# Kernel tuning notes

Measured on AMD Instinct MI355X. Metric: run time of the kernel, lower is better.

## Reference

```python
import jax, jax.numpy as jnp
import numpy as np
from jax import lax

NUM_HEADS = 4
NUM_GROUPS = 32
EPS = 1e-5


def group_norm(x, gamma, beta):
    # x: [b, c, t]
    b, c, t = x.shape
    xg = x.reshape(b, NUM_GROUPS, c // NUM_GROUPS, t)
    mu = jnp.mean(xg, axis=(2, 3), keepdims=True)
    var = jnp.var(xg, axis=(2, 3), keepdims=True)
    xg = (xg - mu) * lax.rsqrt(var + EPS)
    x = xg.reshape(b, c, t)
    return x * gamma[None, :, None] + beta[None, :, None]


def conv1d_same(x, w, b):
    # x: [b, c_in, t], w: [c_out, c_in, k] -> TF-style SAME padding, stride 1
    k = w.shape[-1]
    left = (k - 1) // 2
    right = (k - 1) - left
    y = lax.conv_general_dilated(x, w, window_strides=(1,),
                                 padding=[(left, right)],
                                 dimension_numbers=('NCH', 'OIH', 'NCH'))
    return y + b[None, :, None]


def qkv_attention(qkv):
    # qkv: [b*heads, 3*ch, t]
    ch = qkv.shape[1] // 3
    q, k, v = jnp.split(qkv, 3, axis=1)
    scale = float(ch) ** -0.25  # 1/sqrt(sqrt(ch)) applied to both q and k
    w = jnp.einsum('bct,bcs->bts', q * scale, k * scale)
    w = jax.nn.softmax(w.astype(jnp.float32), axis=-1).astype(qkv.dtype)
    return jnp.einsum('bts,bcs->bct', w, v)


def setup_inputs() -> dict:
    key = jax.random.key(0)
    ks = jax.random.split(key, 5)
    B, C, H, W = 4, 512, 64, 64
    x = jax.random.normal(ks[0], (B, C, H, W), dtype=jnp.float32)
    gn_gamma = jnp.ones((C,), dtype=jnp.float32)
    gn_beta = jnp.zeros((C,), dtype=jnp.float32)
    qkv_w = jax.random.normal(ks[1], (3 * C, C, C // 16), dtype=jnp.float32) * 0.02
    qkv_b = jax.random.normal(ks[2], (3 * C,), dtype=jnp.float32) * 0.02
    proj_w = jax.random.normal(ks[3], (C, C, 5), dtype=jnp.float32) * 0.02
    proj_b = jax.random.normal(ks[4], (C,), dtype=jnp.float32) * 0.02
    return {"x": x, "gn_gamma": gn_gamma, "gn_beta": gn_beta,
            "qkv_w": qkv_w, "qkv_b": qkv_b, "proj_w": proj_w, "proj_b": proj_b}


def reference(x, gn_gamma, gn_beta, qkv_w, qkv_b, proj_w, proj_b):
    b, c = x.shape[0], x.shape[1]
    spatial = x.shape[2:]
    t = int(np.prod(spatial))
    xf = x.reshape(b, c, t)
    qkv = conv1d_same(group_norm(xf, gn_gamma, gn_beta), qkv_w, qkv_b)  # [b, 3c, t]
    qkv = qkv.reshape(b * NUM_HEADS, -1, t)
    h = qkv_attention(qkv)               # [b*heads, c//heads, t]
    h = h.reshape(b, -1, t)              # [b, c, t]
    h = conv1d_same(h, proj_w, proj_b)
    return (xf + h).reshape(b, c, *spatial)
```

## Files before the change

kernel.cpp:

```cpp
#include <hip/hip_runtime.h>
#include <hip/hip_bf16.h>
#include <math.h>

typedef __attribute__((ext_vector_type(8))) __bf16 bf16x8;
typedef __attribute__((ext_vector_type(4))) float  f32x4;

__device__ __forceinline__ unsigned short f2bf(float f) {
    union { float f; unsigned int u; } x; x.f = f;
    unsigned int r = x.u + 0x7fffu + ((x.u >> 16) & 1u);
    return (unsigned short)(r >> 16);
}

__device__ __forceinline__ void gl_lds16(const unsigned short* g, unsigned short* l) {
    auto gp = (const unsigned int __attribute__((address_space(1)))*)((const void*)g);
    auto lp = (unsigned int __attribute__((address_space(3)))*)(unsigned int)(unsigned long long)((void*)l);
    __builtin_amdgcn_global_load_lds(gp, lp, 16, 0, 0);
}

#define B_   4
#define C_   512
#define T_   4096
#define NH   4
#define DH   128

__global__ __launch_bounds__(256) void cvt_wqkv(const float* __restrict__ w, unsigned short* __restrict__ o) {
    __shared__ unsigned short l[512 * 33];
    int co = blockIdx.x;
    const float* src = w + (size_t)co * 16384;
    for (int j = 0; j < 64; j++) {
        int i = threadIdx.x + j * 256;
        l[(i >> 5) * 33 + (i & 31)] = f2bf(src[i]);
    }
    __syncthreads();
    unsigned short* dst = o + (size_t)co * 16384;
    for (int j = 0; j < 64; j++) {
        int i = threadIdx.x + j * 256;
        int dk = i >> 9, ci = i & 511;
        dst[i] = l[ci * 33 + dk];
    }
}

__global__ __launch_bounds__(256) void cvt_wproj(const float* __restrict__ w, unsigned short* __restrict__ o) {
    __shared__ unsigned short l[512 * 6];
    int co = blockIdx.x;
    const float* src = w + (size_t)co * 2560;
    for (int j = 0; j < 10; j++) {
        int i = threadIdx.x + j * 256;
        int ci = i / 5, dk = i - ci * 5;
        l[ci * 6 + dk] = f2bf(src[i]);
    }
    __syncthreads();
    unsigned short* dst = o + (size_t)co * 2560;
    for (int j = 0; j < 10; j++) {
        int i = threadIdx.x + j * 256;
        int dk = i >> 9, ci = i & 511;
        dst[i] = l[ci * 6 + dk];
    }
}

__global__ __launch_bounds__(1024) void groupnorm(const float* __restrict__ x,
                                                  const float* __restrict__ gamma,
                                                  const float* __restrict__ beta,
                                                  unsigned short* __restrict__ gnT) {
    int g = blockIdx.x, b = blockIdx.y;
    int tid = threadIdx.x;
    const float* base = x + ((size_t)b * C_ + g * 16) * T_;
    float s = 0.f, s2 = 0.f;
    const float4* b4 = (const float4*)base;
    for (int j = 0; j < 16; j++) {
        float4 v = b4[tid + j * 1024];
        s  += v.x + v.y + v.z + v.w;
        s2 += v.x * v.x + v.y * v.y + v.z * v.z + v.w * v.w;
    }
    for (int off = 32; off; off >>= 1) { s += __shfl_down(s, off, 64); s2 += __shfl_down(s2, off, 64); }
    __shared__ float red[34];
    int wid = tid >> 6, lane = tid & 63;
    if (lane == 0) { red[wid] = s; red[16 + wid] = s2; }
    __syncthreads();
    if (tid == 0) {
        float ts = 0.f, ts2 = 0.f;
        for (int i = 0; i < 16; i++) { ts += red[i]; ts2 += red[16 + i]; }
        float mu = ts / 65536.f;
        float var = ts2 / 65536.f - mu * mu;
        red[32] = mu; red[33] = rsqrtf(var + 1e-5f);
    }
    __syncthreads();
    float mu = red[32], inv = red[33];
    for (int p = 0; p < 4; p++) {
        int t = tid + p * 1024;
        unsigned short outv[16];
        for (int cc = 0; cc < 16; cc++) {
            float xv = base[(size_t)cc * T_ + t];
            int c = g * 16 + cc;
            outv[cc] = f2bf((xv - mu) * inv * gamma[c] + beta[c]);
        }
        unsigned short* dst = gnT + ((size_t)b * T_ + t) * C_ + g * 16;
        *(uint4*)dst       = *(uint4*)outv;
        *(uint4*)(dst + 8) = *(uint4*)(outv + 8);
    }
}

__global__ __launch_bounds__(256, 3) void gemm_qkv(const unsigned short* __restrict__ gnT,
                                                   const unsigned short* __restrict__ wq,
                                                   const float* __restrict__ bias,
                                                   unsigned short* __restrict__ qT,
                                                   unsigned short* __restrict__ kT,
                                                   unsigned short* __restrict__ vv) {
    int nblk = blockIdx.x, mblk = blockIdx.y, b = blockIdx.z;
    int m0 = mblk * 128, t0 = nblk * 128;
    __shared__ unsigned short As[128 * 64];
    __shared__ unsigned short Bs[128 * 64];
    int tid = threadIdx.x, lane = tid & 63, wave = tid >> 6;
    int quad = lane >> 4, l16 = lane & 15;
    int wm = wave & 1, wn = wave >> 1;

    int srow8 = lane >> 3;
    int scb = (lane & 7) ^ srow8;
    const unsigned short* gb = gnT + (size_t)b * T_ * C_;
    const unsigned short* ap[4]; const unsigned short* bp[4];
    unsigned short *la[4], *lb[4];
#pragma unroll
    for (int i = 0; i < 4; i++) {
        int g = wave * 4 + i;
        int row = g * 8 + srow8;
        ap[i] = wq + (size_t)(m0 + row) * 16384 + scb * 8;
        bp[i] = gb + ((size_t)(t0 - 15 + row)) * 512 + scb * 8;
        la[i] = As + g * 512;
        lb[i] = Bs + g * 512;
    }
    const unsigned short* pAr[2]; const unsigned short* pBr[2];
#pragma unroll
    for (int kk = 0; kk < 2; kk++) {
        pAr[kk] = As + (wm * 64 + l16) * 64 + (((kk * 4 + quad) ^ (l16 & 7)) << 3);
        pBr[kk] = Bs + (wn * 64 + l16) * 64 + (((kk * 4 + quad) ^ (l16 & 7)) << 3);
    }
    f32x4 acc[4][4];
    f32x4 z4 = {0.f, 0.f, 0.f, 0.f};
#pragma unroll
    for (int mt = 0; mt < 4; mt++)
#pragma unroll
        for (int nt = 0; nt < 4; nt++) acc[mt][nt] = z4;

    bool isF = (nblk == 0), isL = (nblk == 31);
    for (int s = 0; s < 256; s++) {
        __syncthreads();
#pragma unroll
        for (int i = 0; i < 4; i++) { gl_lds16(ap[i], la[i]); ap[i] += 64; }
#pragma unroll
        for (int i = 0; i < 4; i++) { gl_lds16(bp[i], lb[i]); bp[i] += 64; }
        __syncthreads();
        int dk = s >> 3;
        if (isF && dk < 15) {
            int nz = 15 - dk, r = tid >> 3;
            if (r < nz) *(uint4*)&Bs[(r << 6) + ((tid & 7) << 3)] = make_uint4(0, 0, 0, 0);
            __syncthreads();
        }
        if (isL && dk > 15) {
            int nb = dk - 15, rr = tid >> 3;
            if (rr < nb) *(uint4*)&Bs[((128 - nb + rr) << 6) + ((tid & 7) << 3)] = make_uint4(0, 0, 0, 0);
            __syncthreads();
        }
#pragma unroll
        for (int kk = 0; kk < 2; kk++) {
            bf16x8 af[4], bfr[4];
#pragma unroll
            for (int mt = 0; mt < 4; mt++) af[mt]  = *(const bf16x8*)(pAr[kk] + mt * 1024);
#pragma unroll
            for (int nt = 0; nt < 4; nt++) bfr[nt] = *(const bf16x8*)(pBr[kk] + nt * 1024);
#pragma unroll
            for (int mt = 0; mt < 4; mt++)
#pragma unroll
                for (int nt = 0; nt < 4; nt++)
                    acc[mt][nt] = __builtin_amdgcn_mfma_f32_16x16x32_bf16(af[mt], bfr[nt], acc[mt][nt], 0, 0, 0);
        }
    }
#pragma unroll
    for (int mt = 0; mt < 4; mt++) {
        int cobase = m0 + wm * 64 + mt * 16 + quad * 4;
        int h = cobase / 384;
        int local = cobase - h * 384;
        int bh = b * NH + h;
#pragma unroll
        for (int nt = 0; nt < 4; nt++) {
            int t = t0 + wn * 64 + nt * 16 + l16;
            f32x4 a = acc[mt][nt];
            unsigned short r4[4];
            for (int r = 0; r < 4; r++) r4[r] = f2bf(a[r] + bias[cobase + r]);
            if (local < 128) {
                unsigned short* dst = qT + ((size_t)bh * T_ + t) * DH + local;
                *(uint2*)dst = *(uint2*)r4;
            } else if (local < 256) {
                unsigned short* dst = kT + ((size_t)bh * T_ + t) * DH + (local - 128);
                *(uint2*)dst = *(uint2*)r4;
            } else {
                unsigned short* dst = vv + ((size_t)bh * DH + (local - 256)) * T_ + t;
                for (int r = 0; r < 4; r++) dst[(size_t)r * T_] = r4[r];
            }
        }
    }
}

__global__ __launch_bounds__(256, 3) void attn(const unsigned short* __restrict__ qT,
                                               const unsigned short* __restrict__ kT,
                                               const unsigned short* __restrict__ vv,
                                               unsigned short* __restrict__ hT) {
    int q0 = blockIdx.x * 64, bh = blockIdx.y;
    int b = bh >> 2, h = bh & 3;
    __shared__ unsigned short Ks[64 * 128];
    __shared__ unsigned short Vs[128 * 64];
    __shared__ unsigned short Ps[64 * 72];
    int tid = threadIdx.x, lane = tid & 63, wave = tid >> 6, quad = lane >> 4, l16 = lane & 15;

    bf16x8 bq[4];
    {
        const unsigned short* qrow = qT + ((size_t)bh * T_ + q0 + wave * 16 + l16) * DH + quad * 8;
#pragma unroll
        for (int kk = 0; kk < 4; kk++) bq[kk] = *(const bf16x8*)(qrow + kk * 32);
    }

    const unsigned short* kbase = kT + (size_t)bh * T_ * DH;
    const unsigned short* vbase = vv + (size_t)bh * DH * T_;
    int krow_in = lane >> 4, kp = lane & 15;
    int vrow_in = lane >> 3, vp = lane & 7;

    float m_i = -1e30f, l_i = 0.f;
    f32x4 z4 = {0.f, 0.f, 0.f, 0.f};
    f32x4 o[8];
#pragma unroll
    for (int nt = 0; nt < 8; nt++) o[nt] = z4;
    const float scale2 = 0.08838834764831845f;

    for (int ts0 = 0; ts0 < T_; ts0 += 64) {
        __syncthreads();
#pragma unroll
        for (int i = 0; i < 4; i++) {
            int row = (wave * 4 + i) * 4 + krow_in;
            gl_lds16(kbase + ((size_t)(ts0 + row)) * DH + (((kp ^ (row & 7)) << 3)),
                     Ks + (wave * 4 + i) * 512);
        }
#pragma unroll
        for (int i = 0; i < 4; i++) {
            int row = (wave * 4 + i) * 8 + vrow_in;
            gl_lds16(vbase + (size_t)row * T_ + ts0 + (((vp ^ (row & 7)) << 3)),
                     Vs + (wave * 4 + i) * 512);
        }
        __syncthreads();

        f32x4 s[4];
#pragma unroll
        for (int mt = 0; mt < 4; mt++) s[mt] = z4;
#pragma unroll
        for (int kk = 0; kk < 4; kk++) {
            int pb = (((kk * 4 + quad) ^ (l16 & 7)) << 3);
#pragma unroll
            for (int mt = 0; mt < 4; mt++) {
                bf16x8 ak = *(const bf16x8*)&Ks[(mt * 16 + l16) * 128 + pb];
                s[mt] = __builtin_amdgcn_mfma_f32_16x16x32_bf16(ak, bq[kk], s[mt], 0, 0, 0);
            }
        }
        float mx = -1e30f;
#pragma unroll
        for (int mt = 0; mt < 4; mt++) {
            s[mt] *= scale2;
            mx = fmaxf(mx, fmaxf(fmaxf(s[mt][0], s[mt][1]), fmaxf(s[mt][2], s[mt][3])));
        }
        mx = fmaxf(mx, __shfl_xor(mx, 16, 64));
        mx = fmaxf(mx, __shfl_xor(mx, 32, 64));
        float mnew = fmaxf(m_i, mx);
        float alpha = __expf(m_i - mnew);
        float rs = 0.f;
#pragma unroll
        for (int mt = 0; mt < 4; mt++) {
#pragma unroll
            for (int r = 0; r < 4; r++) { float p = __expf(s[mt][r] - mnew); s[mt][r] = p; rs += p; }
        }
        rs += __shfl_xor(rs, 16, 64);
        rs += __shfl_xor(rs, 32, 64);
        m_i = mnew;
        l_i = l_i * alpha + rs;
#pragma unroll
        for (int mt = 0; mt < 4; mt++) {
            unsigned short t4[4];
#pragma unroll
            for (int r = 0; r < 4; r++) t4[r] = f2bf(s[mt][r]);
            *(uint2*)&Ps[(wave * 16 + l16) * 72 + mt * 16 + quad * 4] = *(uint2*)t4;
        }
        float a0 = __shfl(alpha, quad * 4 + 0, 64);
        float a1 = __shfl(alpha, quad * 4 + 1, 64);
        float a2 = __shfl(alpha, quad * 4 + 2, 64);
        float a3 = __shfl(alpha, quad * 4 + 3, 64);
        f32x4 av = {a0, a1, a2, a3};
#pragma unroll
        for (int nt = 0; nt < 8; nt++) o[nt] *= av;
#pragma unroll
        for (int kk = 0; kk < 2; kk++) {
            bf16x8 ap = *(const bf16x8*)&Ps[(wave * 16 + l16) * 72 + kk * 32 + quad * 8];
            int pb = (((kk * 4 + quad) ^ (l16 & 7)) << 3);
#pragma unroll
            for (int nt = 0; nt < 8; nt++) {
                bf16x8 bv = *(const bf16x8*)&Vs[(nt * 16 + l16) * 64 + pb];
                o[nt] = __builtin_amdgcn_mfma_f32_16x16x32_bf16(ap, bv, o[nt], 0, 0, 0);
            }
        }
    }
    float i0 = 1.f / __shfl(l_i, quad * 4 + 0, 64);
    float i1 = 1.f / __shfl(l_i, quad * 4 + 1, 64);
    float i2 = 1.f / __shfl(l_i, quad * 4 + 2, 64);
    float i3 = 1.f / __shfl(l_i, quad * 4 + 3, 64);
    f32x4 iv = {i0, i1, i2, i3};
#pragma unroll
    for (int r = 0; r < 4; r++) {
        int t = q0 + wave * 16 + quad * 4 + r;
        unsigned short* dst = hT + ((size_t)b * T_ + t) * C_ + h * DH;
#pragma unroll
        for (int nt = 0; nt < 8; nt++) dst[nt * 16 + l16] = f2bf(o[nt][r] * iv[r]);
    }
}

__global__ __launch_bounds__(256, 3) void gemm_proj(const unsigned short* __restrict__ hT,
                                                    const unsigned short* __restrict__ wp,
                                                    const float* __restrict__ bias,
                                                    const float* __restrict__ x,
                                                    float* __restrict__ out) {
    int nblk = blockIdx.x, mblk = blockIdx.y, b = blockIdx.z;
    int m0 = mblk * 128, t0 = nblk * 128;
    __shared__ unsigned short As[128 * 64], Bs[128 * 64];
    int tid = threadIdx.x, lane = tid & 63, wave = tid >> 6;
    int quad = lane >> 4, l16 = lane & 15;
    int wm = wave & 1, wn = wave >> 1;

    int srow8 = lane >> 3;
    int scb = (lane & 7) ^ srow8;
    const unsigned short* hb = hT + (size_t)b * T_ * C_;
    const unsigned short* ap[4]; const unsigned short* bp[4];
    unsigned short *la[4], *lb[4];
#pragma unroll
    for (int i = 0; i < 4; i++) {
        int g = wave * 4 + i;
        int row = g * 8 + srow8;
        ap[i] = wp + (size_t)(m0 + row) * 2560 + scb * 8;
        bp[i] = hb + ((size_t)(t0 - 2 + row)) * 512 + scb * 8;
        la[i] = As + g * 512;
        lb[i] = Bs + g * 512;
    }
    const unsigned short* pAr[2]; const unsigned short* pBr[2];
#pragma unroll
    for (int kk = 0; kk < 2; kk++) {
        pAr[kk] = As + (wm * 64 + l16) * 64 + (((kk * 4 + quad) ^ (l16 & 7)) << 3);
        pBr[kk] = Bs + (wn * 64 + l16) * 64 + (((kk * 4 + quad) ^ (l16 & 7)) << 3);
    }
    f32x4 acc[4][4];
    f32x4 z4 = {0.f, 0.f, 0.f, 0.f};
#pragma unroll
    for (int mt = 0; mt < 4; mt++)
#pragma unroll
        for (int nt = 0; nt < 4; nt++) acc[mt][nt] = z4;

    bool isF = (nblk == 0), isL = (nblk == 31);
    for (int s = 0; s < 40; s++) {
        __syncthreads();
#pragma unroll
        for (int i = 0; i < 4; i++) { gl_lds16(ap[i], la[i]); ap[i] += 64; }
#pragma unroll
        for (int i = 0; i < 4; i++) { gl_lds16(bp[i], lb[i]); bp[i] += 64; }
        __syncthreads();
        int dk = s >> 3;
        if (isF && dk < 2) {
            int nz = 2 - dk, r = tid >> 3;
            if (r < nz) *(uint4*)&Bs[(r << 6) + ((tid & 7) << 3)] = make_uint4(0, 0, 0, 0);
            __syncthreads();
        }
        if (isL && dk > 2) {
            int nb = dk - 2, rr = tid >> 3;
            if (rr < nb) *(uint4*)&Bs[((128 - nb + rr) << 6) + ((tid & 7) << 3)] = make_uint4(0, 0, 0, 0);
            __syncthreads();
        }
#pragma unroll
        for (int kk = 0; kk < 2; kk++) {
            bf16x8 af[4], bfr[4];
#pragma unroll
            for (int mt = 0; mt < 4; mt++) af[mt]  = *(const bf16x8*)(pAr[kk] + mt * 1024);
#pragma unroll
            for (int nt = 0; nt < 4; nt++) bfr[nt] = *(const bf16x8*)(pBr[kk] + nt * 1024);
#pragma unroll
            for (int mt = 0; mt < 4; mt++)
#pragma unroll
                for (int nt = 0; nt < 4; nt++)
                    acc[mt][nt] = __builtin_amdgcn_mfma_f32_16x16x32_bf16(af[mt], bfr[nt], acc[mt][nt], 0, 0, 0);
        }
    }
#pragma unroll
    for (int mt = 0; mt < 4; mt++) {
        int cobase = m0 + wm * 64 + mt * 16 + quad * 4;
#pragma unroll
        for (int nt = 0; nt < 4; nt++) {
            int t = t0 + wn * 64 + nt * 16 + l16;
            for (int r = 0; r < 4; r++) {
                int co = cobase + r;
                size_t idx = ((size_t)(b * C_ + co)) * T_ + t;
                out[idx] = acc[mt][nt][r] + bias[co] + x[idx];
            }
        }
    }
}

extern "C" void kernel_launch(void* const* d_in, const int* in_sizes, int n_in,
                              void* d_out, int out_size, void* d_ws, size_t ws_size,
                              hipStream_t stream) {
    const float* x      = (const float*)d_in[0];
    const float* gamma  = (const float*)d_in[1];
    const float* beta   = (const float*)d_in[2];
    const float* qkv_w  = (const float*)d_in[3];
    const float* qkv_b  = (const float*)d_in[4];
    const float* proj_w = (const float*)d_in[5];
    const float* proj_b = (const float*)d_in[6];
    float* out = (float*)d_out;
    char* ws = (char*)d_ws;

    unsigned short* wqkvT  = (unsigned short*)(ws);
    unsigned short* wprojT = (unsigned short*)(ws + 50331648);
    unsigned short* gnT    = (unsigned short*)(ws + 52953088);
    unsigned short* qTb    = (unsigned short*)(ws + 69730304);
    unsigned short* kTb    = (unsigned short*)(ws + 86507520);
    unsigned short* vb     = (unsigned short*)(ws + 103284736);
    unsigned short* hT     = gnT;

    hipLaunchKernelGGL(cvt_wqkv,  dim3(1536),      dim3(256),  0, stream, qkv_w, wqkvT);
    hipLaunchKernelGGL(cvt_wproj, dim3(512),       dim3(256),  0, stream, proj_w, wprojT);
    hipLaunchKernelGGL(groupnorm, dim3(32, 4),     dim3(1024), 0, stream, x, gamma, beta, gnT);
    hipLaunchKernelGGL(gemm_qkv,  dim3(32, 12, 4), dim3(256),  0, stream, gnT, wqkvT, qkv_b, qTb, kTb, vb);
    hipLaunchKernelGGL(attn,      dim3(64, 16),    dim3(256),  0, stream, qTb, kTb, vb, hT);
    hipLaunchKernelGGL(gemm_proj, dim3(32, 4, 4),  dim3(256),  0, stream, hT, wprojT, proj_b, x, out);
}
```

Measured before the change: 1.268 ms.

## Double-buffer GEMM LDS tiles and process two query tiles per attention wave

The two conv GEMMs now use double-buffered shared-memory tiles, so the next K-slice's global-to-LDS load is issued before the current slice's MFMAs and one barrier per step is dropped. Grid indexing is flattened so batch and time blocks share the x dimension. The attention kernel gives each wave 32 query rows (two 16-row tiles), so each K/V tile in LDS is reused across 128 queries per block and fewer blocks reload K/V. The cost is more LDS and registers, with occupancy bounds lowered from 3 to 2. The async load into the other buffer also relies on the single barrier per iteration for correctness, including around the boundary zero-fill writes.

Result: slower. 1.371 ms (+8.1%).

```diff
diff --git a/kernel.cpp b/kernel.cpp
--- a/kernel.cpp
+++ b/kernel.cpp
@@ -100,16 +100,16 @@
     }
 }
 
-__global__ __launch_bounds__(256, 3) void gemm_qkv(const unsigned short* __restrict__ gnT,
+__global__ __launch_bounds__(256, 2) void gemm_qkv(const unsigned short* __restrict__ gnT,
                                                    const unsigned short* __restrict__ wq,
                                                    const float* __restrict__ bias,
                                                    unsigned short* __restrict__ qT,
                                                    unsigned short* __restrict__ kT,
                                                    unsigned short* __restrict__ vv) {
-    int nblk = blockIdx.x, mblk = blockIdx.y, b = blockIdx.z;
+    int nblk = blockIdx.x & 31, b = blockIdx.x >> 5, mblk = blockIdx.y;
     int m0 = mblk * 128, t0 = nblk * 128;
-    __shared__ unsigned short As[128 * 64];
-    __shared__ unsigned short Bs[128 * 64];
+    __shared__ unsigned short As[2][128 * 64];
+    __shared__ unsigned short Bs[2][128 * 64];
     int tid = threadIdx.x, lane = tid & 63, wave = tid >> 6;
     int quad = lane >> 4, l16 = lane & 15;
     int wm = wave & 1, wn = wave >> 1;
@@ -118,22 +118,18 @@
     int scb = (lane & 7) ^ srow8;
     const unsigned short* gb = gnT + (size_t)b * T_ * C_;
     const unsigned short* ap[4]; const unsigned short* bp[4];
-    unsigned short *la[4], *lb[4];
+    int lo[4];
 #pragma unroll
     for (int i = 0; i < 4; i++) {
         int g = wave * 4 + i;
         int row = g * 8 + srow8;
         ap[i] = wq + (size_t)(m0 + row) * 16384 + scb * 8;
         bp[i] = gb + ((size_t)(t0 - 15 + row)) * 512 + scb * 8;
-        la[i] = As + g * 512;
-        lb[i] = Bs + g * 512;
-    }
-    const unsigned short* pAr[2]; const unsigned short* pBr[2];
-#pragma unroll
-    for (int kk = 0; kk < 2; kk++) {
-        pAr[kk] = As + (wm * 64 + l16) * 64 + (((kk * 4 + quad) ^ (l16 & 7)) << 3);
-        pBr[kk] = Bs + (wn * 64 + l16) * 64 + (((kk * 4 + quad) ^ (l16 & 7)) << 3);
-    }
+        lo[i] = g * 512;
+    }
+    int fo[2];
+#pragma unroll
+    for (int kk = 0; kk < 2; kk++) fo[kk] = (((kk * 4 + quad) ^ (l16 & 7)) << 3);
     f32x4 acc[4][4];
     f32x4 z4 = {0.f, 0.f, 0.f, 0.f};
 #pragma unroll
@@ -142,31 +138,39 @@
         for (int nt = 0; nt < 4; nt++) acc[mt][nt] = z4;
 
     bool isF = (nblk == 0), isL = (nblk == 31);
+#pragma unroll
+    for (int i = 0; i < 4; i++) { gl_lds16(ap[i], &As[0][lo[i]]); ap[i] += 64; }
+#pragma unroll
+    for (int i = 0; i < 4; i++) { gl_lds16(bp[i], &Bs[0][lo[i]]); bp[i] += 64; }
+
     for (int s = 0; s < 256; s++) {
+        int cur = s & 1;
         __syncthreads();
-#pragma unroll
-        for (int i = 0; i < 4; i++) { gl_lds16(ap[i], la[i]); ap[i] += 64; }
-#pragma unroll
-        for (int i = 0; i < 4; i++) { gl_lds16(bp[i], lb[i]); bp[i] += 64; }
-        __syncthreads();
+        if (s != 255) {
+            int nx = cur ^ 1;
+#pragma unroll
+            for (int i = 0; i < 4; i++) { gl_lds16(ap[i], &As[nx][lo[i]]); ap[i] += 64; }
+#pragma unroll
+            for (int i = 0; i < 4; i++) { gl_lds16(bp[i], &Bs[nx][lo[i]]); bp[i] += 64; }
+        }
         int dk = s >> 3;
         if (isF && dk < 15) {
             int nz = 15 - dk, r = tid >> 3;
-            if (r < nz) *(uint4*)&Bs[(r << 6) + ((tid & 7) << 3)] = make_uint4(0, 0, 0, 0);
+            if (r < nz) *(uint4*)&Bs[cur][(r << 6) + ((tid & 7) << 3)] = make_uint4(0, 0, 0, 0);
             __syncthreads();
         }
         if (isL && dk > 15) {
             int nb = dk - 15, rr = tid >> 3;
-            if (rr < nb) *(uint4*)&Bs[((128 - nb + rr) << 6) + ((tid & 7) << 3)] = make_uint4(0, 0, 0, 0);
+            if (rr < nb) *(uint4*)&Bs[cur][((128 - nb + rr) << 6) + ((tid & 7) << 3)] = make_uint4(0, 0, 0, 0);
             __syncthreads();
         }
 #pragma unroll
         for (int kk = 0; kk < 2; kk++) {
             bf16x8 af[4], bfr[4];
 #pragma unroll
-            for (int mt = 0; mt < 4; mt++) af[mt]  = *(const bf16x8*)(pAr[kk] + mt * 1024);
-#pragma unroll
-            for (int nt = 0; nt < 4; nt++) bfr[nt] = *(const bf16x8*)(pBr[kk] + nt * 1024);
+            for (int mt = 0; mt < 4; mt++) af[mt]  = *(const bf16x8*)&As[cur][(wm * 64 + mt * 16 + l16) * 64 + fo[kk]];
+#pragma unroll
+            for (int nt = 0; nt < 4; nt++) bfr[nt] = *(const bf16x8*)&Bs[cur][(wn * 64 + nt * 16 + l16) * 64 + fo[kk]];
 #pragma unroll
             for (int mt = 0; mt < 4; mt++)
 #pragma unroll
@@ -200,22 +204,23 @@
     }
 }
 
-__global__ __launch_bounds__(256, 3) void attn(const unsigned short* __restrict__ qT,
+__global__ __launch_bounds__(256, 2) void attn(const unsigned short* __restrict__ qT,
                                                const unsigned short* __restrict__ kT,
                                                const unsigned short* __restrict__ vv,
                                                unsigned short* __restrict__ hT) {
-    int q0 = blockIdx.x * 64, bh = blockIdx.y;
+    int q0 = blockIdx.x * 128, bh = blockIdx.y;
     int b = bh >> 2, h = bh & 3;
     __shared__ unsigned short Ks[64 * 128];
     __shared__ unsigned short Vs[128 * 64];
-    __shared__ unsigned short Ps[64 * 72];
+    __shared__ unsigned short Ps[128 * 72];
     int tid = threadIdx.x, lane = tid & 63, wave = tid >> 6, quad = lane >> 4, l16 = lane & 15;
 
-    bf16x8 bq[4];
-    {
-        const unsigned short* qrow = qT + ((size_t)bh * T_ + q0 + wave * 16 + l16) * DH + quad * 8;
-#pragma unroll
-        for (int kk = 0; kk < 4; kk++) bq[kk] = *(const bf16x8*)(qrow + kk * 32);
+    bf16x8 bq[2][4];
+#pragma unroll
+    for (int u = 0; u < 2; u++) {
+        const unsigned short* qrow = qT + ((size_t)bh * T_ + q0 + wave * 32 + u * 16 + l16) * DH + quad * 8;
+#pragma unroll
+        for (int kk = 0; kk < 4; kk++) bq[u][kk] = *(const bf16x8*)(qrow + kk * 32);
     }
 
     const unsigned short* kbase = kT + (size_t)bh * T_ * DH;
@@ -223,11 +228,13 @@
     int krow_in = lane >> 4, kp = lane & 15;
     int vrow_in = lane >> 3, vp = lane & 7;
 
-    float m_i = -1e30f, l_i = 0.f;
+    float m_i[2] = {-1e30f, -1e30f}, l_i[2] = {0.f, 0.f};
     f32x4 z4 = {0.f, 0.f, 0.f, 0.f};
-    f32x4 o[8];
-#pragma unroll
-    for (int nt = 0; nt < 8; nt++) o[nt] = z4;
+    f32x4 o[2][8];
+#pragma unroll
+    for (int u = 0; u < 2; u++)
+#pragma unroll
+        for (int nt = 0; nt < 8; nt++) o[u][nt] = z4;
     const float scale2 = 0.08838834764831845f;
 
     for (int ts0 = 0; ts0 < T_; ts0 += 64) {
@@ -246,85 +253,96 @@
         }
         __syncthreads();
 
-        f32x4 s[4];
-#pragma unroll
-        for (int mt = 0; mt < 4; mt++) s[mt] = z4;
+        f32x4 s[2][4];
+#pragma unroll
+        for (int u = 0; u < 2; u++)
+#pragma unroll
+            for (int mt = 0; mt < 4; mt++) s[u][mt] = z4;
 #pragma unroll
         for (int kk = 0; kk < 4; kk++) {
             int pb = (((kk * 4 + quad) ^ (l16 & 7)) << 3);
 #pragma unroll
             for (int mt = 0; mt < 4; mt++) {
                 bf16x8 ak = *(const bf16x8*)&Ks[(mt * 16 + l16) * 128 + pb];
-                s[mt] = __builtin_amdgcn_mfma_f32_16x16x32_bf16(ak, bq[kk], s[mt], 0, 0, 0);
-            }
-        }
-        float mx = -1e30f;
-#pragma unroll
-        for (int mt = 0; mt < 4; mt++) {
-            s[mt] *= scale2;
-            mx = fmaxf(mx, fmaxf(fmaxf(s[mt][0], s[mt][1]), fmaxf(s[mt][2], s[mt][3])));
-        }
-        mx = fmaxf(mx, __shfl_xor(mx, 16, 64));
-        mx = fmaxf(mx, __shfl_xor(mx, 32, 64));
-        float mnew = fmaxf(m_i, mx);
-        float alpha = __expf(m_i - mnew);
-        float rs = 0.f;
-#pragma unroll
-        for (int mt = 0; mt < 4; mt++) {
-#pragma unroll
-            for (int r = 0; r < 4; r++) { float p = __expf(s[mt][r] - mnew); s[mt][r] = p; rs += p; }
-        }
-        rs += __shfl_xor(rs, 16, 64);
-        rs += __shfl_xor(rs, 32, 64);
-        m_i = mnew;
-        l_i = l_i * alpha + rs;
-#pragma unroll
-        for (int mt = 0; mt < 4; mt++) {
-            unsigned short t4[4];
-#pragma unroll
-            for (int r = 0; r < 4; r++) t4[r] = f2bf(s[mt][r]);
-            *(uint2*)&Ps[(wave * 16 + l16) * 72 + mt * 16 + quad * 4] = *(uint2*)t4;
-        }
-        float a0 = __shfl(alpha, quad * 4 + 0, 64);
-        float a1 = __shfl(alpha, quad * 4 + 1, 64);
-        float a2 = __shfl(alpha, quad * 4 + 2, 64);
-        float a3 = __shfl(alpha, quad * 4 + 3, 64);
-        f32x4 av = {a0, a1, a2, a3};
-#pragma unroll
-        for (int nt = 0; nt < 8; nt++) o[nt] *= av;
+                s[0][mt] = __builtin_amdgcn_mfma_f32_16x16x32_bf16(ak, bq[0][kk], s[0][mt], 0, 0, 0);
+                s[1][mt] = __builtin_amdgcn_mfma_f32_16x16x32_bf16(ak, bq[1][kk], s[1][mt], 0, 0, 0);
+            }
+        }
+#pragma unroll
+        for (int u = 0; u < 2; u++) {
+            float mx = -1e30f;
+#pragma unroll
+            for (int mt = 0; mt < 4; mt++) {
+                s[u][mt] *= scale2;
+                mx = fmaxf(mx, fmaxf(fmaxf(s[u][mt][0], s[u][mt][1]), fmaxf(s[u][mt][2], s[u][mt][3])));
+            }
+            mx = fmaxf(mx, __shfl_xor(mx, 16, 64));
+            mx = fmaxf(mx, __shfl_xor(mx, 32, 64));
+            float mnew = fmaxf(m_i[u], mx);
+            float alpha = __expf(m_i[u] - mnew);
+            float rs = 0.f;
+#pragma unroll
+            for (int mt = 0; mt < 4; mt++) {
+#pragma unroll
+                for (int r = 0; r < 4; r++) { float p = __expf(s[u][mt][r] - mnew); s[u][mt][r] = p; rs += p; }
+            }
+            rs += __shfl_xor(rs, 16, 64);
+            rs += __shfl_xor(rs, 32, 64);
+            m_i[u] = mnew;
+            l_i[u] = l_i[u] * alpha + rs;
+#pragma unroll
+            for (int mt = 0; mt < 4; mt++) {
+                unsigned short t4[4];
+#pragma unroll
+                for (int r = 0; r < 4; r++) t4[r] = f2bf(s[u][mt][r]);
+                *(uint2*)&Ps[(wave * 32 + u * 16 + l16) * 72 + mt * 16 + quad * 4] = *(uint2*)t4;
+            }
+            float a0 = __shfl(alpha, quad * 4 + 0, 64);
+            float a1 = __shfl(alpha, quad * 4 + 1, 64);
+            float a2 = __shfl(alpha, quad * 4 + 2, 64);
+            float a3 = __shfl(alpha, quad * 4 + 3, 64);
+            f32x4 av = {a0, a1, a2, a3};
+#pragma unroll
+            for (int nt = 0; nt < 8; nt++) o[u][nt] *= av;
+        }
 #pragma unroll
         for (int kk = 0; kk < 2; kk++) {
-            bf16x8 ap = *(const bf16x8*)&Ps[(wave * 16 + l16) * 72 + kk * 32 + quad * 8];
             int pb = (((kk * 4 + quad) ^ (l16 & 7)) << 3);
+            bf16x8 ap0 = *(const bf16x8*)&Ps[(wave * 32 + l16) * 72 + kk * 32 + quad * 8];
+            bf16x8 ap1 = *(const bf16x8*)&Ps[(wave * 32 + 16 + l16) * 72 + kk * 32 + quad * 8];
 #pragma unroll
             for (int nt = 0; nt < 8; nt++) {
                 bf16x8 bv = *(const bf16x8*)&Vs[(nt * 16 + l16) * 64 + pb];
-                o[nt] = __builtin_amdgcn_mfma_f32_16x16x32_bf16(ap, bv, o[nt], 0, 0, 0);
-            }
-        }
-    }
-    float i0 = 1.f / __shfl(l_i, quad * 4 + 0, 64);
-    float i1 = 1.f / __shfl(l_i, quad * 4 + 1, 64);
-    float i2 = 1.f / __shfl(l_i, quad * 4 + 2, 64);
-    float i3 = 1.f / __shfl(l_i, quad * 4 + 3, 64);
-    f32x4 iv = {i0, i1, i2, i3};
-#pragma unroll
-    for (int r = 0; r < 4; r++) {
-        int t = q0 + wave * 16 + quad * 4 + r;
-        unsigned short* dst = hT + ((size_t)b * T_ + t) * C_ + h * DH;
-#pragma unroll
-        for (int nt = 0; nt < 8; nt++) dst[nt * 16 + l16] = f2bf(o[nt][r] * iv[r]);
-    }
-}
-
-__global__ __launch_bounds__(256, 3) void gemm_proj(const unsigned short* __restrict__ hT,
+                o[0][nt] = __builtin_amdgcn_mfma_f32_16x16x32_bf16(ap0, bv, o[0][nt], 0, 0, 0);
+                o[1][nt] = __builtin_amdgcn_mfma_f32_16x16x32_bf16(ap1, bv, o[1][nt], 0, 0, 0);
+            }
+        }
+    }
+#pragma unroll
+    for (int u = 0; u < 2; u++) {
+        float i0 = 1.f / __shfl(l_i[u], quad * 4 + 0, 64);
+        float i1 = 1.f / __shfl(l_i[u], quad * 4 + 1, 64);
+        float i2 = 1.f / __shfl(l_i[u], quad * 4 + 2, 64);
+        float i3 = 1.f / __shfl(l_i[u], quad * 4 + 3, 64);
+        f32x4 iv = {i0, i1, i2, i3};
+#pragma unroll
+        for (int r = 0; r < 4; r++) {
+            int t = q0 + wave * 32 + u * 16 + quad * 4 + r;
+            unsigned short* dst = hT + ((size_t)b * T_ + t) * C_ + h * DH;
+#pragma unroll
+            for (int nt = 0; nt < 8; nt++) dst[nt * 16 + l16] = f2bf(o[u][nt][r] * iv[r]);
+        }
+    }
+}
+
+__global__ __launch_bounds__(256, 2) void gemm_proj(const unsigned short* __restrict__ hT,
                                                     const unsigned short* __restrict__ wp,
                                                     const float* __restrict__ bias,
                                                     const float* __restrict__ x,
                                                     float* __restrict__ out) {
-    int nblk = blockIdx.x, mblk = blockIdx.y, b = blockIdx.z;
+    int nblk = blockIdx.x & 31, b = blockIdx.x >> 5, mblk = blockIdx.y;
     int m0 = mblk * 128, t0 = nblk * 128;
-    __shared__ unsigned short As[128 * 64], Bs[128 * 64];
+    __shared__ unsigned short As[2][128 * 64], Bs[2][128 * 64];
     int tid = threadIdx.x, lane = tid & 63, wave = tid >> 6;
     int quad = lane >> 4, l16 = lane & 15;
     int wm = wave & 1, wn = wave >> 1;
@@ -333,22 +351,18 @@
     int scb = (lane & 7) ^ srow8;
     const unsigned short* hb = hT + (size_t)b * T_ * C_;
     const unsigned short* ap[4]; const unsigned short* bp[4];
-    unsigned short *la[4], *lb[4];
+    int lo[4];
 #pragma unroll
     for (int i = 0; i < 4; i++) {
         int g = wave * 4 + i;
         int row = g * 8 + srow8;
         ap[i] = wp + (size_t)(m0 + row) * 2560 + scb * 8;
         bp[i] = hb + ((size_t)(t0 - 2 + row)) * 512 + scb * 8;
-        la[i] = As + g * 512;
-        lb[i] = Bs + g * 512;
-    }
-    const unsigned short* pAr[2]; const unsigned short* pBr[2];
-#pragma unroll
-    for (int kk = 0; kk < 2; kk++) {
-        pAr[kk] = As + (wm * 64 + l16) * 64 + (((kk * 4 + quad) ^ (l16 & 7)) << 3);
-        pBr[kk] = Bs + (wn * 64 + l16) * 64 + (((kk * 4 + quad) ^ (l16 & 7)) << 3);
-    }
+        lo[i] = g * 512;
+    }
+    int fo[2];
+#pragma unroll
+    for (int kk = 0; kk < 2; kk++) fo[kk] = (((kk * 4 + quad) ^ (l16 & 7)) << 3);
     f32x4 acc[4][4];
     f32x4 z4 = {0.f, 0.f, 0.f, 0.f};
 #pragma unroll
@@ -357,31 +371,39 @@
         for (int nt = 0; nt < 4; nt++) acc[mt][nt] = z4;
 
     bool isF = (nblk == 0), isL = (nblk == 31);
+#pragma unroll
+    for (int i = 0; i < 4; i++) { gl_lds16(ap[i], &As[0][lo[i]]); ap[i] += 64; }
+#pragma unroll
+    for (int i = 0; i < 4; i++) { gl_lds16(bp[i], &Bs[0][lo[i]]); bp[i] += 64; }
+
     for (int s = 0; s < 40; s++) {
+        int cur = s & 1;
         __syncthreads();
-#pragma unroll
-        for (int i = 0; i < 4; i++) { gl_lds16(ap[i], la[i]); ap[i] += 64; }
-#pragma unroll
-        for (int i = 0; i < 4; i++) { gl_lds16(bp[i], lb[i]); bp[i] += 64; }
-        __syncthreads();
+        if (s != 39) {
+            int nx = cur ^ 1;
+#pragma unroll
+            for (int i = 0; i < 4; i++) { gl_lds16(ap[i], &As[nx][lo[i]]); ap[i] += 64; }
+#pragma unroll
+            for (int i = 0; i < 4; i++) { gl_lds16(bp[i], &Bs[nx][lo[i]]); bp[i] += 64; }
+        }
         int dk = s >> 3;
         if (isF && dk < 2) {
             int nz = 2 - dk, r = tid >> 3;
-            if (r < nz) *(uint4*)&Bs[(r << 6) + ((tid & 7) << 3)] = make_uint4(0, 0, 0, 0);
+            if (r < nz) *(uint4*)&Bs[cur][(r << 6) + ((tid & 7) << 3)] = make_uint4(0, 0, 0, 0);
             __syncthreads();
         }
         if (isL && dk > 2) {
             int nb = dk - 2, rr = tid >> 3;
-            if (rr < nb) *(uint4*)&Bs[((128 - nb + rr) << 6) + ((tid & 7) << 3)] = make_uint4(0, 0, 0, 0);
+            if (rr < nb) *(uint4*)&Bs[cur][((128 - nb + rr) << 6) + ((tid & 7) << 3)] = make_uint4(0, 0, 0, 0);
             __syncthreads();
         }
 #pragma unroll
         for (int kk = 0; kk < 2; kk++) {
             bf16x8 af[4], bfr[4];
 #pragma unroll
-            for (int mt = 0; mt < 4; mt++) af[mt]  = *(const bf16x8*)(pAr[kk] + mt * 1024);
-#pragma unroll
-            for (int nt = 0; nt < 4; nt++) bfr[nt] = *(const bf16x8*)(pBr[kk] + nt * 1024);
+            for (int mt = 0; mt < 4; mt++) af[mt]  = *(const bf16x8*)&As[cur][(wm * 64 + mt * 16 + l16) * 64 + fo[kk]];
+#pragma unroll
+            for (int nt = 0; nt < 4; nt++) bfr[nt] = *(const bf16x8*)&Bs[cur][(wn * 64 + nt * 16 + l16) * 64 + fo[kk]];
 #pragma unroll
             for (int mt = 0; mt < 4; mt++)
 #pragma unroll
@@ -425,10 +447,10 @@
     unsigned short* vb     = (unsigned short*)(ws + 103284736);
     unsigned short* hT     = gnT;
 
-    hipLaunchKernelGGL(cvt_wqkv,  dim3(1536),      dim3(256),  0, stream, qkv_w, wqkvT);
-    hipLaunchKernelGGL(cvt_wproj, dim3(512),       dim3(256),  0, stream, proj_w, wprojT);
-    hipLaunchKernelGGL(groupnorm, dim3(32, 4),     dim3(1024), 0, stream, x, gamma, beta, gnT);
-    hipLaunchKernelGGL(gemm_qkv,  dim3(32, 12, 4), dim3(256),  0, stream, gnT, wqkvT, qkv_b, qTb, kTb, vb);
-    hipLaunchKernelGGL(attn,      dim3(64, 16),    dim3(256),  0, stream, qTb, kTb, vb, hT);
-    hipLaunchKernelGGL(gemm_proj, dim3(32, 4, 4),  dim3(256),  0, stream, hT, wprojT, proj_b, x, out);
-}
+    hipLaunchKernelGGL(cvt_wqkv,  dim3(1536),     dim3(256),  0, stream, qkv_w, wqkvT);
+    hipLaunchKernelGGL(cvt_wproj, dim3(512),      dim3(256),  0, stream, proj_w, wprojT);
+    hipLaunchKernelGGL(groupnorm, dim3(32, 4),    dim3(1024), 0, stream, x, gamma, beta, gnT);
+    hipLaunchKernelGGL(gemm_qkv,  dim3(128, 12),  dim3(256),  0, stream, gnT, wqkvT, qkv_b, qTb, kTb, vb);
+    hipLaunchKernelGGL(attn,      dim3(32, 16),   dim3(256),  0, stream, qTb, kTb, vb, hT);
+    hipLaunchKernelGGL(gemm_proj, dim3(128, 4),   dim3(256),  0, stream, hT, wprojT, proj_b, x, out);
+}
```
